# Kernel tuning notes

Hardware: AMD Instinct MI355X
Metric: run time of the kernel (lower is better)

The kernel has to match this reference:

```python
import jax, jax.numpy as jnp
import numpy as np

B, S, H = 2, 2048, 1024
NH, NKV, HD = 16, 16, 64
R, KF = 16, 4
THETA = 1000000.0


def setup_inputs() -> dict:
    key = jax.random.key(0)
    ks = jax.random.split(key, 16)
    sc = 0.02
    signs = jax.random.randint(ks[13], (1, 1, 1, KF, HD // 2), 0, 2).astype(jnp.float32) * 2 - 1
    cdma = jnp.concatenate([signs, signs], axis=-1)  # [1,1,1,KF,HD]
    return {
        "hidden_states": jax.random.normal(ks[0], (B, S, H), jnp.float32),
        "position_ids": jnp.broadcast_to(jnp.arange(S, dtype=jnp.int32), (B, S)),
        "q_w": jax.random.normal(ks[1], (H, H), jnp.float32) * sc,
        "q_b": jax.random.normal(ks[2], (H,), jnp.float32) * sc,
        "k_w": jax.random.normal(ks[3], (H, H), jnp.float32) * sc,
        "k_b": jax.random.normal(ks[4], (H,), jnp.float32) * sc,
        "v_w": jax.random.normal(ks[5], (H, H), jnp.float32) * sc,
        "v_b": jax.random.normal(ks[6], (H,), jnp.float32) * sc,
        "o_w": jax.random.normal(ks[7], (H, H), jnp.float32) * sc,
        "lora_qA": jax.random.normal(ks[8], (R, H), jnp.float32) * sc,
        "lora_qB": jax.random.normal(ks[9], (H, R), jnp.float32) * sc,
        "lora_vA": jax.random.normal(ks[10], (R, H), jnp.float32) * sc,
        "lora_vB": jax.random.normal(ks[11], (H, R), jnp.float32) * sc,
        "cdma_keys": cdma,
    }


def _rope(q, k, position_ids):
    # cos/sin per HF rotary embedding, theta=1e6 (Qwen1.5)
    inv_freq = 1.0 / (THETA ** (jnp.arange(0, HD, 2, dtype=jnp.float32) / HD))  # [HD/2]
    freqs = position_ids.astype(jnp.float32)[..., None] * inv_freq  # [B,S,HD/2]
    emb = jnp.concatenate([freqs, freqs], axis=-1)  # [B,S,HD]
    cos = jnp.cos(emb)[:, None]  # [B,1,S,HD]
    sin = jnp.sin(emb)[:, None]

    def rot_half(x):
        return jnp.concatenate([-x[..., HD // 2:], x[..., :HD // 2]], axis=-1)

    return q * cos + rot_half(q) * sin, k * cos + rot_half(k) * sin


def reference(hidden_states, position_ids, q_w, q_b, k_w, k_b, v_w, v_b, o_w,
              lora_qA, lora_qB, lora_vA, lora_vB, cdma_keys):
    bsz, q_len, _ = hidden_states.shape
    # base projections + LoRA adjustments (k has no LoRA)
    q = hidden_states @ q_w.T + q_b + (hidden_states @ lora_qA.T) @ lora_qB.T
    k = hidden_states @ k_w.T + k_b
    v = hidden_states @ v_w.T + v_b + (hidden_states @ lora_vA.T) @ lora_vB.T

    q = q.reshape(bsz, q_len, NH, HD).transpose(0, 2, 1, 3)   # [B,NH,S,HD]
    k = k.reshape(bsz, q_len, NKV, HD).transpose(0, 2, 1, 3)  # [B,NKV,S,HD]
    v = v.reshape(bsz, q_len, NKV, HD).transpose(0, 2, 1, 3)

    q, k = _rope(q, k, position_ids)

    # holographic block sign-bind/sum transform (q_len divisible by KF -> no pad)
    n_slots = q_len // KF
    k_blocks = k.reshape(bsz, NKV, n_slots, KF, HD)
    v_blocks = v.reshape(bsz, NKV, n_slots, KF, HD)
    S_K = jnp.sum(k_blocks * cdma_keys, axis=3, keepdims=True)  # [B,NKV,slots,1,HD]
    S_V = jnp.sum(v_blocks * cdma_keys, axis=3, keepdims=True)
    K_noisy = (S_K * cdma_keys).reshape(bsz, NKV, q_len, HD)
    V_noisy = (S_V * cdma_keys).reshape(bsz, NKV, q_len, HD)

    scale = 1.0 / (np.sqrt(HD) * np.sqrt(KF))
    scores = jnp.einsum('bhqd,bhkd->bhqk', q, K_noisy) * scale
    causal = jnp.tril(jnp.ones((q_len, q_len), dtype=bool))
    scores = jnp.where(causal, scores, jnp.float32(-1e9))
    attn = jax.nn.softmax(scores, axis=-1)
    out = jnp.einsum('bhqk,bhkd->bhqd', attn, V_noisy)
    out = out.transpose(0, 2, 1, 3).reshape(bsz, q_len, NH * HD)
    return out @ o_w.T
```

## Files before the change

kernel.cpp:

```cpp
#include <hip/hip_runtime.h>
#include <hip/hip_bf16.h>
#include <math.h>


typedef __bf16 bf16;
typedef __attribute__((ext_vector_type(8))) __bf16 bf16x8;
typedef __attribute__((ext_vector_type(4))) float f32x4;

#define NB 2
#define SEQ 2048
#define HID 1024
#define NHD 16
#define HDD 64

__device__ __forceinline__ void gld_lds16(const void* g, void* l) {
  __builtin_amdgcn_global_load_lds(
      (const __attribute__((address_space(1))) void*)g,
      (__attribute__((address_space(3))) void*)l, 16, 0, 0);
}

__device__ __forceinline__ unsigned pack2bf(float a, float b) {
  unsigned short ua = __builtin_bit_cast(unsigned short, (bf16)a);
  unsigned short ub = __builtin_bit_cast(unsigned short, (bf16)b);
  return ((unsigned)ub << 16) | ua;
}

__global__ __launch_bounds__(256) void prep_wqkv(
    const float* __restrict__ qw, const float* __restrict__ kw,
    const float* __restrict__ vw, const float* __restrict__ qA,
    const float* __restrict__ qB, const float* __restrict__ vA,
    const float* __restrict__ vB, bf16* __restrict__ W) {
  int idx = blockIdx.x * 256 + threadIdx.x;
  if (idx >= 3072 * 1024) return;
  int n = idx >> 10, k = idx & 1023;
  float v;
  if (n < 1024) {
    v = qw[n * 1024 + k];
#pragma unroll
    for (int r = 0; r < 16; ++r) v += qB[n * 16 + r] * qA[r * 1024 + k];
  } else if (n < 2048) {
    v = kw[(n - 1024) * 1024 + k];
  } else {
    int nn = n - 2048;
    v = vw[nn * 1024 + k];
#pragma unroll
    for (int r = 0; r < 16; ++r) v += vB[nn * 16 + r] * vA[r * 1024 + k];
  }
  int seg = k >> 6, cl = k & 63;
  int ch = (cl >> 3) ^ (n & 7);
  W[(size_t)n * 1024 + (seg << 6) + (ch << 3) + (cl & 7)] = (bf16)v;
}

__global__ __launch_bounds__(256) void cvt_swz(const float* __restrict__ src,
                                               bf16* __restrict__ dst,
                                               int total, int cols) {
  int idx = blockIdx.x * 256 + threadIdx.x;
  if (idx >= total) return;
  int r = idx / cols, c = idx - r * cols;
  int seg = c >> 6, cl = c & 63;
  int ch = (cl >> 3) ^ (r & 7);
  dst[(size_t)r * cols + (seg << 6) + (ch << 3) + (cl & 7)] = (bf16)src[idx];
}

__global__ void bias_cat(const float* __restrict__ qb, const float* __restrict__ kb,
                         const float* __restrict__ vb, float* __restrict__ out) {
  int i = blockIdx.x * 256 + threadIdx.x;
  if (i >= 3072) return;
  out[i] = (i < 1024) ? qb[i] : (i < 2048 ? kb[i - 1024] : vb[i - 2048]);
}

__global__ void rope_tab(float* __restrict__ ct, float* __restrict__ st) {
  int idx = blockIdx.x * 256 + threadIdx.x;
  if (idx >= SEQ * 32) return;
  int s = idx >> 5, i = idx & 31;
  double inv = pow(1.0e6, -(double)i / 32.0);
  double a = (double)s * inv;
  ct[idx] = (float)cos(a);
  st[idx] = (float)sin(a);
}

__global__ __launch_bounds__(256) void gemm_bt(
    const bf16* __restrict__ A, const bf16* __restrict__ Bw,
    const float* __restrict__ bias, bf16* __restrict__ Cb,
    float* __restrict__ Cf, int M, int N, int K) {
  __shared__ __align__(16) bf16 As[128 * 64];
  __shared__ __align__(16) bf16 Bs[128 * 64];
  const int tid = threadIdx.x;
  const int lane = tid & 63, w = tid >> 6;
  const int wm = w >> 1, wn = w & 1;
  const int l15 = lane & 15, l4 = lane >> 4;
  const int m0 = blockIdx.y * 128, n0 = blockIdx.x * 128;
  const size_t rowb = (size_t)K * 2;
  const char* gA = (const char*)A + (size_t)m0 * rowb;
  const char* gB = (const char*)Bw + (size_t)n0 * rowb;
  f32x4 acc[4][4] = {};

  for (int k0 = 0; k0 < K; k0 += 64) {
    const char* gAk = gA + k0 * 2;
    const char* gBk = gB + k0 * 2;
#pragma unroll
    for (int i = 0; i < 4; ++i) {
      int idx = i * 256 + tid;
      int row = idx >> 3, ch = idx & 7;
      gld_lds16(gAk + (size_t)row * rowb + ch * 16,
                (char*)As + (i * 256 + (w << 6)) * 16);
      gld_lds16(gBk + (size_t)row * rowb + ch * 16,
                (char*)Bs + (i * 256 + (w << 6)) * 16);
    }
    __syncthreads();
#pragma unroll
    for (int c = 0; c < 2; ++c) {
      bf16x8 af[4], bfr[4];
#pragma unroll
      for (int mi = 0; mi < 4; ++mi) {
        int row = wm * 64 + mi * 16 + l15;
        int ch = (c * 4 + l4) ^ (row & 7);
        af[mi] = *(const bf16x8*)(As + row * 64 + ch * 8);
      }
#pragma unroll
      for (int ni = 0; ni < 4; ++ni) {
        int row = wn * 64 + ni * 16 + l15;
        int ch = (c * 4 + l4) ^ (row & 7);
        bfr[ni] = *(const bf16x8*)(Bs + row * 64 + ch * 8);
      }
#pragma unroll
      for (int mi = 0; mi < 4; ++mi)
#pragma unroll
        for (int ni = 0; ni < 4; ++ni)
          acc[mi][ni] = __builtin_amdgcn_mfma_f32_16x16x32_bf16(
              af[mi], bfr[ni], acc[mi][ni], 0, 0, 0);
    }
    __syncthreads();
  }
#pragma unroll
  for (int mi = 0; mi < 4; ++mi) {
    int rbase = m0 + wm * 64 + mi * 16 + l4 * 4;
#pragma unroll
    for (int ni = 0; ni < 4; ++ni) {
      int col = n0 + wn * 64 + ni * 16 + l15;
      float badd = bias ? bias[col] : 0.0f;
#pragma unroll
      for (int r = 0; r < 4; ++r) {
        float v = acc[mi][ni][r] + badd;
        if (Cf) Cf[(size_t)(rbase + r) * N + col] = v;
        else    Cb[(size_t)(rbase + r) * N + col] = (bf16)v;
      }
    }
  }
}

__global__ __launch_bounds__(256) void rope_q(
    const bf16* __restrict__ qkv, const int* __restrict__ pos,
    const float* __restrict__ ct, const float* __restrict__ st,
    bf16* __restrict__ Qr) {
  const float SCQ = 0.0901684403f;
  int idx = blockIdx.x * 256 + threadIdx.x;
  if (idx >= NB * NHD * SEQ * 32) return;
  int i = idx & 31, h = (idx >> 5) & 15, s = (idx >> 9) & 2047, b = idx >> 20;
  int p = pos[b * SEQ + s];
  float co = ct[p * 32 + i], sn = st[p * 32 + i];
  size_t base = ((size_t)(b * SEQ + s)) * 3072 + h * 64 + i;
  float x = (float)qkv[base], y = (float)qkv[base + 32];
  size_t ob = ((size_t)((b * 16 + h) * SEQ + s)) * 64 + i;
  Qr[ob]      = (bf16)((x * co - y * sn) * SCQ);
  Qr[ob + 32] = (bf16)((y * co + x * sn) * SCQ);
}

__global__ __launch_bounds__(256) void holo_kv(
    const bf16* __restrict__ qkv, const int* __restrict__ pos,
    const float* __restrict__ ct, const float* __restrict__ st,
    const float* __restrict__ cdma, bf16* __restrict__ Kn,
    bf16* __restrict__ Vt) {
  int idx = blockIdx.x * 256 + threadIdx.x;
  if (idx >= NB * NHD * (SEQ / 4) * 32) return;
  int i = idx & 31, slot = (idx >> 5) & 511, h = (idx >> 14) & 15, b = idx >> 18;
  float c[4];
  float SK = 0.f, SK2 = 0.f, SV = 0.f, SV2 = 0.f;
#pragma unroll
  for (int f = 0; f < 4; ++f) {
    int s = slot * 4 + f;
    float cf = cdma[f * 64 + i];
    c[f] = cf;
    size_t base = ((size_t)(b * SEQ + s)) * 3072 + h * 64 + i;
    float kx = (float)qkv[base + 1024], ky = (float)qkv[base + 1024 + 32];
    int p = pos[b * SEQ + s];
    float co = ct[p * 32 + i], sn = st[p * 32 + i];
    SK  += (kx * co - ky * sn) * cf;
    SK2 += (ky * co + kx * sn) * cf;
    SV  += (float)qkv[base + 2048] * cf;
    SV2 += (float)qkv[base + 2048 + 32] * cf;
  }
  size_t hb = (size_t)(b * 16 + h);
#pragma unroll
  for (int f = 0; f < 4; ++f) {
    int s = slot * 4 + f;
    size_t krow = (hb * SEQ + s) * 64;
    int ch0 = (i >> 3) ^ (s & 7);
    int ch1 = (4 + (i >> 3)) ^ (s & 7);
    Kn[krow + ch0 * 8 + (i & 7)] = (bf16)(SK * c[f]);
    Kn[krow + ch1 * 8 + (i & 7)] = (bf16)(SK2 * c[f]);
    int seg = s >> 6, cl = s & 63;
    int vch = (cl >> 3) ^ (i & 7);
    size_t vrow0 = (hb * 64 + i) * (size_t)SEQ + (seg << 6);
    size_t vrow1 = (hb * 64 + i + 32) * (size_t)SEQ + (seg << 6);
    Vt[vrow0 + vch * 8 + (cl & 7)] = (bf16)(SV * c[f]);
    Vt[vrow1 + vch * 8 + (cl & 7)] = (bf16)(SV2 * c[f]);
  }
}

__global__ __launch_bounds__(256) void attn_fwd(
    const bf16* __restrict__ Qr, const bf16* __restrict__ Kn,
    const bf16* __restrict__ Vt, bf16* __restrict__ AO) {
  __shared__ __align__(16) bf16 Kt[2][128 * 64];
  __shared__ __align__(16) bf16 Vl[2][64 * 128];
  __shared__ __align__(16) bf16 Pt[4][16 * 128];
  const int pq = blockIdx.x, h = blockIdx.y, b = blockIdx.z;
  const int tid = threadIdx.x, lane = tid & 63, w = tid >> 6;
  const int l15 = lane & 15, l4 = lane >> 4;
  const size_t hd = ((size_t)(b * 16 + h)) * SEQ * 64;
  const char* gK0 = (const char*)(Kn + hd);
  const char* gV0 = (const char*)(Vt + hd);
  char* pw = (char*)&Pt[w][0];

#pragma unroll 1
  for (int phase = 0; phase < 2; ++phase) {
    const int qt = phase ? (31 - pq) : pq;
    const int q0 = qt * 64;
    const int qg = q0 + w * 16 + l15;
    const int nt = (qt >> 1) + 1;

    const bf16* qb = Qr + hd + (size_t)qg * 64;
    bf16x8 qf0 = *(const bf16x8*)(qb + l4 * 8);
    bf16x8 qf1 = *(const bf16x8*)(qb + 32 + l4 * 8);

    f32x4 oacc[4] = {};
    float m = -1e30f, lsum = 0.0f;

#pragma unroll
    for (int i = 0; i < 4; ++i)
      gld_lds16(gK0 + (i * 256 + tid) * 16,
                (char*)Kt[0] + (i * 256 + (w << 6)) * 16);
#pragma unroll
    for (int i = 0; i < 4; ++i) {
      int idx = i * 256 + tid;
      int row = idx >> 4, ch = idx & 15;
      gld_lds16(gV0 + (size_t)row * (SEQ * 2) + ch * 16,
                (char*)Vl[0] + (i * 256 + (w << 6)) * 16);
    }

#pragma unroll 1
    for (int t = 0; t < nt; ++t) {
      const int cur = t & 1;
      if (t + 1 < nt) {
        const int tn = t + 1, sb = cur ^ 1;
#pragma unroll
        for (int i = 0; i < 4; ++i)
          gld_lds16(gK0 + (size_t)tn * 16384 + (i * 256 + tid) * 16,
                    (char*)Kt[sb] + (i * 256 + (w << 6)) * 16);
#pragma unroll
        for (int i = 0; i < 4; ++i) {
          int idx = i * 256 + tid;
          int row = idx >> 4, ch = idx & 15;
          gld_lds16(gV0 + (size_t)row * (SEQ * 2) + tn * 256 + ch * 16,
                    (char*)Vl[sb] + (i * 256 + (w << 6)) * 16);
        }
        asm volatile("s_waitcnt vmcnt(8)\ns_barrier" ::: "memory");
      } else {
        asm volatile("s_waitcnt vmcnt(0)\ns_barrier" ::: "memory");
      }

      const bf16* Ktc = Kt[cur];
      const bf16* Vlc = Vl[cur];
      const int kv0 = t * 128;
      const bool lastt = (t == nt - 1);

      f32x4 sacc[8] = {};
#pragma unroll
      for (int c = 0; c < 2; ++c) {
        bf16x8 qf = c ? qf1 : qf0;
#pragma unroll
        for (int nf = 0; nf < 8; ++nf) {
          int row = nf * 16 + l15;
          int ch = (c * 4 + l4) ^ (row & 7);
          bf16x8 kf = *(const bf16x8*)(Ktc + row * 64 + ch * 8);
          sacc[nf] = __builtin_amdgcn_mfma_f32_16x16x32_bf16(kf, qf, sacc[nf], 0, 0, 0);
        }
      }

      float pmax = -1e30f;
      if (lastt) {
#pragma unroll
        for (int nf = 0; nf < 8; ++nf)
#pragma unroll
          for (int r = 0; r < 4; ++r) {
            int kvg = kv0 + nf * 16 + l4 * 4 + r;
            float v = (kvg > qg) ? -1e30f : sacc[nf][r];
            sacc[nf][r] = v;
            pmax = fmaxf(pmax, v);
          }
      } else {
#pragma unroll
        for (int nf = 0; nf < 8; ++nf)
#pragma unroll
          for (int r = 0; r < 4; ++r) pmax = fmaxf(pmax, sacc[nf][r]);
      }
      pmax = fmaxf(pmax, __shfl_xor(pmax, 16));
      pmax = fmaxf(pmax, __shfl_xor(pmax, 32));

      if (!__all(pmax <= m)) {
        float mn = fmaxf(m, pmax);
        float al = exp2f(m - mn);
        m = mn;
        lsum *= al;
#pragma unroll
        for (int df = 0; df < 4; ++df) oacc[df] *= al;
      }
      float rs = 0.0f;
#pragma unroll
      for (int nf = 0; nf < 8; ++nf)
#pragma unroll
        for (int r = 0; r < 4; ++r) {
          float e = exp2f(sacc[nf][r] - m);
          sacc[nf][r] = e;
          rs += e;
        }
      rs += __shfl_xor(rs, 16);
      rs += __shfl_xor(rs, 32);
      lsum += rs;

#pragma unroll
      for (int nf = 0; nf < 8; ++nf)
#pragma unroll
        for (int rp = 0; rp < 2; ++rp) {
          unsigned u = pack2bf(sacc[nf][rp * 2], sacc[nf][rp * 2 + 1]);
          int boff = l15 * 256 + nf * 32 + l4 * 8 + rp * 4;
          boff ^= (l15 & 7) << 4;
          *(unsigned*)(pw + boff) = u;
        }

#pragma unroll
      for (int c2 = 0; c2 < 4; ++c2) {
        int pb = (l15 * 256 + c2 * 64 + l4 * 16) ^ ((l15 & 7) << 4);
        bf16x8 pf = *(const bf16x8*)(pw + pb);
        int vbyte = (c2 * 64 + l4 * 16) ^ ((l15 & 7) << 4);
#pragma unroll
        for (int df = 0; df < 4; ++df) {
          int vrow = df * 16 + l15;
          bf16x8 vf = *(const bf16x8*)((const char*)Vlc + vrow * 256 + vbyte);
          oacc[df] = __builtin_amdgcn_mfma_f32_16x16x32_bf16(vf, pf, oacc[df], 0, 0, 0);
        }
      }
      asm volatile("s_barrier" ::: "memory");
    }

    const float li = 1.0f / lsum;
    const size_t arow = ((size_t)(b * SEQ + qg)) * HID + h * 64;
    const int qk7 = qg & 7;
#pragma unroll
    for (int df = 0; df < 4; ++df)
#pragma unroll
      for (int r = 0; r < 4; ++r) {
        int d = df * 16 + l4 * 4 + r;
        int ch = (d >> 3) ^ qk7;
        AO[arow + ch * 8 + (d & 7)] = (bf16)(oacc[df][r] * li);
      }
  }
}

extern "C" void kernel_launch(void* const* d_in, const int* in_sizes, int n_in,
                              void* d_out, int out_size, void* d_ws, size_t ws_size,
                              hipStream_t stream) {
  const float* hs  = (const float*)d_in[0];
  const int* pos   = (const int*)d_in[1];
  const float* qw  = (const float*)d_in[2];
  const float* qb_ = (const float*)d_in[3];
  const float* kw  = (const float*)d_in[4];
  const float* kb_ = (const float*)d_in[5];
  const float* vw  = (const float*)d_in[6];
  const float* vb_ = (const float*)d_in[7];
  const float* ow  = (const float*)d_in[8];
  const float* qA  = (const float*)d_in[9];
  const float* qB  = (const float*)d_in[10];
  const float* vA  = (const float*)d_in[11];
  const float* vB  = (const float*)d_in[12];
  const float* cd  = (const float*)d_in[13];

  char* p = (char*)d_ws;
  auto alloc = [&](size_t bytes) {
    char* r = p; p += (bytes + 255) & ~(size_t)255; return r;
  };
  bf16* hsb   = (bf16*)alloc((size_t)4096 * 1024 * 2);
  bf16* Wqkv  = (bf16*)alloc((size_t)3072 * 1024 * 2);
  float* bqkv = (float*)alloc(3072 * 4);
  bf16* owb   = (bf16*)alloc((size_t)1024 * 1024 * 2);
  bf16* qkvb  = (bf16*)alloc((size_t)4096 * 3072 * 2);
  float* ct   = (float*)alloc((size_t)SEQ * 32 * 4);
  float* st   = (float*)alloc((size_t)SEQ * 32 * 4);
  bf16* Qrb   = (bf16*)alloc((size_t)NB * NHD * SEQ * 64 * 2);
  bf16* Knb   = (bf16*)alloc((size_t)NB * NHD * SEQ * 64 * 2);
  bf16* Vtb   = (bf16*)alloc((size_t)NB * NHD * 64 * SEQ * 2);
  bf16* AOb   = (bf16*)alloc((size_t)4096 * 1024 * 2);

  prep_wqkv<<<dim3(3072 * 1024 / 256), 256, 0, stream>>>(qw, kw, vw, qA, qB, vA, vB, Wqkv);
  cvt_swz<<<dim3(4096 * 1024 / 256), 256, 0, stream>>>(hs, hsb, 4096 * 1024, 1024);
  cvt_swz<<<dim3(1024 * 1024 / 256), 256, 0, stream>>>(ow, owb, 1024 * 1024, 1024);
  bias_cat<<<dim3(12), 256, 0, stream>>>(qb_, kb_, vb_, bqkv);
  rope_tab<<<dim3(SEQ * 32 / 256), 256, 0, stream>>>(ct, st);
  gemm_bt<<<dim3(3072 / 128, 4096 / 128), 256, 0, stream>>>(
      hsb, Wqkv, bqkv, qkvb, nullptr, 4096, 3072, 1024);
  rope_q<<<dim3(NB * NHD * SEQ * 32 / 256), 256, 0, stream>>>(qkvb, pos, ct, st, Qrb);
  holo_kv<<<dim3(NB * NHD * (SEQ / 4) * 32 / 256), 256, 0, stream>>>(
      qkvb, pos, ct, st, cd, Knb, Vtb);
  attn_fwd<<<dim3(16, NHD, NB), 256, 0, stream>>>(Qrb, Knb, Vtb, AOb);
  gemm_bt<<<dim3(1024 / 128, 4096 / 128), 256, 0, stream>>>(
      AOb, owb, nullptr, nullptr, (float*)d_out, 4096, 1024, 1024);
}
```

Measured before the change: 166.3 us.

## Merge prep kernels, vectorize rope/holo kernels, split softmax reductions

Folds the five preprocessing kernels (weight merge, two bf16 conversions, bias concat, rope table) into a single launch that branches on block ID. The rope_q and holo_kv kernels now have each thread handle eight contiguous elements with 16-byte bf16x8 loads and stores instead of scalar accesses. In attention, the row max and row sum are accumulated into four independent partials to shorten dependency chains, and probabilities are stored to LDS as 8-byte pairs. The aim is to cut launch overhead and memory-instruction count; the Vt transpose writes stay scalar and strided.

```diff
diff --git a/kernel.cpp b/kernel.cpp
--- a/kernel.cpp
+++ b/kernel.cpp
@@ -6,6 +6,7 @@
 typedef __bf16 bf16;
 typedef __attribute__((ext_vector_type(8))) __bf16 bf16x8;
 typedef __attribute__((ext_vector_type(4))) float f32x4;
+typedef __attribute__((ext_vector_type(2))) unsigned u32x2;
 
 #define NB 2
 #define SEQ 2048
@@ -25,58 +26,65 @@
   return ((unsigned)ub << 16) | ua;
 }
 
-__global__ __launch_bounds__(256) void prep_wqkv(
-    const float* __restrict__ qw, const float* __restrict__ kw,
-    const float* __restrict__ vw, const float* __restrict__ qA,
-    const float* __restrict__ qB, const float* __restrict__ vA,
-    const float* __restrict__ vB, bf16* __restrict__ W) {
-  int idx = blockIdx.x * 256 + threadIdx.x;
-  if (idx >= 3072 * 1024) return;
-  int n = idx >> 10, k = idx & 1023;
-  float v;
-  if (n < 1024) {
-    v = qw[n * 1024 + k];
-#pragma unroll
-    for (int r = 0; r < 16; ++r) v += qB[n * 16 + r] * qA[r * 1024 + k];
-  } else if (n < 2048) {
-    v = kw[(n - 1024) * 1024 + k];
+#define RB_W    12288
+#define RB_HS   (RB_W + 16384)
+#define RB_OW   (RB_HS + 4096)
+#define RB_BIAS (RB_OW + 12)
+#define RB_TAB  (RB_BIAS + 256)
+
+__global__ __launch_bounds__(256) void prep_all(
+    const float* __restrict__ hs, const float* __restrict__ ow,
+    const float* __restrict__ qw, const float* __restrict__ qb,
+    const float* __restrict__ kw, const float* __restrict__ kb,
+    const float* __restrict__ vw, const float* __restrict__ vb,
+    const float* __restrict__ qA, const float* __restrict__ qB,
+    const float* __restrict__ vA, const float* __restrict__ vB,
+    bf16* __restrict__ hsb, bf16* __restrict__ owb, bf16* __restrict__ Wqkv,
+    float* __restrict__ bqkv, float* __restrict__ ct, float* __restrict__ st) {
+  const int bid = blockIdx.x, tid = threadIdx.x;
+  if (bid < RB_W) {
+    int idx = bid * 256 + tid;
+    int n = idx >> 10, k = idx & 1023;
+    float v;
+    if (n < 1024) {
+      v = qw[n * 1024 + k];
+#pragma unroll
+      for (int r = 0; r < 16; ++r) v += qB[n * 16 + r] * qA[r * 1024 + k];
+    } else if (n < 2048) {
+      v = kw[(n - 1024) * 1024 + k];
+    } else {
+      int nn = n - 2048;
+      v = vw[nn * 1024 + k];
+#pragma unroll
+      for (int r = 0; r < 16; ++r) v += vB[nn * 16 + r] * vA[r * 1024 + k];
+    }
+    int seg = k >> 6, cl = k & 63;
+    int ch = (cl >> 3) ^ (n & 7);
+    Wqkv[(size_t)n * 1024 + (seg << 6) + (ch << 3) + (cl & 7)] = (bf16)v;
+  } else if (bid < RB_HS) {
+    int idx = (bid - RB_W) * 256 + tid;
+    int r = idx >> 10, c = idx & 1023;
+    int seg = c >> 6, cl = c & 63;
+    int ch = (cl >> 3) ^ (r & 7);
+    hsb[(size_t)r * 1024 + (seg << 6) + (ch << 3) + (cl & 7)] = (bf16)hs[idx];
+  } else if (bid < RB_OW) {
+    int idx = (bid - RB_HS) * 256 + tid;
+    int r = idx >> 10, c = idx & 1023;
+    int seg = c >> 6, cl = c & 63;
+    int ch = (cl >> 3) ^ (r & 7);
+    owb[(size_t)r * 1024 + (seg << 6) + (ch << 3) + (cl & 7)] = (bf16)ow[idx];
+  } else if (bid < RB_BIAS) {
+    int i = (bid - RB_OW) * 256 + tid;
+    if (i < 3072)
+      bqkv[i] = (i < 1024) ? qb[i] : (i < 2048 ? kb[i - 1024] : vb[i - 2048]);
   } else {
-    int nn = n - 2048;
-    v = vw[nn * 1024 + k];
-#pragma unroll
-    for (int r = 0; r < 16; ++r) v += vB[nn * 16 + r] * vA[r * 1024 + k];
-  }
-  int seg = k >> 6, cl = k & 63;
-  int ch = (cl >> 3) ^ (n & 7);
-  W[(size_t)n * 1024 + (seg << 6) + (ch << 3) + (cl & 7)] = (bf16)v;
-}
-
-__global__ __launch_bounds__(256) void cvt_swz(const float* __restrict__ src,
-                                               bf16* __restrict__ dst,
-                                               int total, int cols) {
-  int idx = blockIdx.x * 256 + threadIdx.x;
-  if (idx >= total) return;
-  int r = idx / cols, c = idx - r * cols;
-  int seg = c >> 6, cl = c & 63;
-  int ch = (cl >> 3) ^ (r & 7);
-  dst[(size_t)r * cols + (seg << 6) + (ch << 3) + (cl & 7)] = (bf16)src[idx];
-}
-
-__global__ void bias_cat(const float* __restrict__ qb, const float* __restrict__ kb,
-                         const float* __restrict__ vb, float* __restrict__ out) {
-  int i = blockIdx.x * 256 + threadIdx.x;
-  if (i >= 3072) return;
-  out[i] = (i < 1024) ? qb[i] : (i < 2048 ? kb[i - 1024] : vb[i - 2048]);
-}
-
-__global__ void rope_tab(float* __restrict__ ct, float* __restrict__ st) {
-  int idx = blockIdx.x * 256 + threadIdx.x;
-  if (idx >= SEQ * 32) return;
-  int s = idx >> 5, i = idx & 31;
-  double inv = pow(1.0e6, -(double)i / 32.0);
-  double a = (double)s * inv;
-  ct[idx] = (float)cos(a);
-  st[idx] = (float)sin(a);
+    int idx = (bid - RB_BIAS) * 256 + tid;
+    int s = idx >> 5, i = idx & 31;
+    double inv = pow(1.0e6, -(double)i / 32.0);
+    double a = (double)s * inv;
+    ct[idx] = (float)cos(a);
+    st[idx] = (float)sin(a);
+  }
 }
 
 __global__ __launch_bounds__(256) void gemm_bt(
@@ -155,15 +163,25 @@
     bf16* __restrict__ Qr) {
   const float SCQ = 0.0901684403f;
   int idx = blockIdx.x * 256 + threadIdx.x;
-  if (idx >= NB * NHD * SEQ * 32) return;
-  int i = idx & 31, h = (idx >> 5) & 15, s = (idx >> 9) & 2047, b = idx >> 20;
+  if (idx >= NB * NHD * SEQ * 4) return;
+  int ih = idx & 3, s = (idx >> 2) & 2047, h = (idx >> 13) & 15, b = idx >> 17;
   int p = pos[b * SEQ + s];
-  float co = ct[p * 32 + i], sn = st[p * 32 + i];
-  size_t base = ((size_t)(b * SEQ + s)) * 3072 + h * 64 + i;
-  float x = (float)qkv[base], y = (float)qkv[base + 32];
-  size_t ob = ((size_t)((b * 16 + h) * SEQ + s)) * 64 + i;
-  Qr[ob]      = (bf16)((x * co - y * sn) * SCQ);
-  Qr[ob + 32] = (bf16)((y * co + x * sn) * SCQ);
+  size_t base = ((size_t)(b * SEQ + s)) * 3072 + h * 64 + ih * 8;
+  bf16x8 xv = *(const bf16x8*)(qkv + base);
+  bf16x8 yv = *(const bf16x8*)(qkv + base + 32);
+  const float* ctp = ct + p * 32 + ih * 8;
+  const float* stp = st + p * 32 + ih * 8;
+  bf16x8 o0, o1;
+#pragma unroll
+  for (int e = 0; e < 8; ++e) {
+    float x = (float)xv[e], y = (float)yv[e];
+    float co = ctp[e], sn = stp[e];
+    o0[e] = (bf16)((x * co - y * sn) * SCQ);
+    o1[e] = (bf16)((y * co + x * sn) * SCQ);
+  }
+  size_t ob = ((size_t)((b * 16 + h) * SEQ + s)) * 64 + ih * 8;
+  *(bf16x8*)(Qr + ob) = o0;
+  *(bf16x8*)(Qr + ob + 32) = o1;
 }
 
 __global__ __launch_bounds__(256) void holo_kv(
@@ -172,39 +190,57 @@
     const float* __restrict__ cdma, bf16* __restrict__ Kn,
     bf16* __restrict__ Vt) {
   int idx = blockIdx.x * 256 + threadIdx.x;
-  if (idx >= NB * NHD * (SEQ / 4) * 32) return;
-  int i = idx & 31, slot = (idx >> 5) & 511, h = (idx >> 14) & 15, b = idx >> 18;
-  float c[4];
-  float SK = 0.f, SK2 = 0.f, SV = 0.f, SV2 = 0.f;
+  if (idx >= NB * NHD * (SEQ / 4) * 4) return;
+  int ih = idx & 3, slot = (idx >> 2) & 511, h = (idx >> 11) & 15, b = idx >> 15;
+  float SK[8] = {}, SK2[8] = {}, SV[8] = {}, SV2[8] = {};
 #pragma unroll
   for (int f = 0; f < 4; ++f) {
     int s = slot * 4 + f;
-    float cf = cdma[f * 64 + i];
-    c[f] = cf;
-    size_t base = ((size_t)(b * SEQ + s)) * 3072 + h * 64 + i;
-    float kx = (float)qkv[base + 1024], ky = (float)qkv[base + 1024 + 32];
+    size_t base = ((size_t)(b * SEQ + s)) * 3072 + h * 64 + ih * 8;
+    bf16x8 klo = *(const bf16x8*)(qkv + base + 1024);
+    bf16x8 khi = *(const bf16x8*)(qkv + base + 1024 + 32);
+    bf16x8 vlo = *(const bf16x8*)(qkv + base + 2048);
+    bf16x8 vhi = *(const bf16x8*)(qkv + base + 2048 + 32);
     int p = pos[b * SEQ + s];
-    float co = ct[p * 32 + i], sn = st[p * 32 + i];
-    SK  += (kx * co - ky * sn) * cf;
-    SK2 += (ky * co + kx * sn) * cf;
-    SV  += (float)qkv[base + 2048] * cf;
-    SV2 += (float)qkv[base + 2048 + 32] * cf;
+    const float* ctp = ct + p * 32 + ih * 8;
+    const float* stp = st + p * 32 + ih * 8;
+    const float* cdp = cdma + f * 64 + ih * 8;
+#pragma unroll
+    for (int e = 0; e < 8; ++e) {
+      float cf = cdp[e];
+      float kx = (float)klo[e], ky = (float)khi[e];
+      float co = ctp[e], sn = stp[e];
+      SK[e]  += (kx * co - ky * sn) * cf;
+      SK2[e] += (ky * co + kx * sn) * cf;
+      SV[e]  += (float)vlo[e] * cf;
+      SV2[e] += (float)vhi[e] * cf;
+    }
   }
   size_t hb = (size_t)(b * 16 + h);
 #pragma unroll
   for (int f = 0; f < 4; ++f) {
     int s = slot * 4 + f;
+    const float* cdp = cdma + f * 64 + ih * 8;
+    bf16x8 k0, k1;
+#pragma unroll
+    for (int e = 0; e < 8; ++e) {
+      k0[e] = (bf16)(SK[e] * cdp[e]);
+      k1[e] = (bf16)(SK2[e] * cdp[e]);
+    }
     size_t krow = (hb * SEQ + s) * 64;
-    int ch0 = (i >> 3) ^ (s & 7);
-    int ch1 = (4 + (i >> 3)) ^ (s & 7);
-    Kn[krow + ch0 * 8 + (i & 7)] = (bf16)(SK * c[f]);
-    Kn[krow + ch1 * 8 + (i & 7)] = (bf16)(SK2 * c[f]);
+    int ch0 = ih ^ (s & 7);
+    int ch1 = (4 + ih) ^ (s & 7);
+    *(bf16x8*)(Kn + krow + ch0 * 8) = k0;
+    *(bf16x8*)(Kn + krow + ch1 * 8) = k1;
     int seg = s >> 6, cl = s & 63;
-    int vch = (cl >> 3) ^ (i & 7);
-    size_t vrow0 = (hb * 64 + i) * (size_t)SEQ + (seg << 6);
-    size_t vrow1 = (hb * 64 + i + 32) * (size_t)SEQ + (seg << 6);
-    Vt[vrow0 + vch * 8 + (cl & 7)] = (bf16)(SV * c[f]);
-    Vt[vrow1 + vch * 8 + (cl & 7)] = (bf16)(SV2 * c[f]);
+    size_t vcol = (size_t)(seg << 6) + (cl & 7);
+#pragma unroll
+    for (int e = 0; e < 8; ++e) {
+      int i = ih * 8 + e;
+      int vch = (cl >> 3) ^ (i & 7);
+      Vt[(hb * 64 + i) * (size_t)SEQ + vcol + vch * 8] = (bf16)(SV[e] * cdp[e]);
+      Vt[(hb * 64 + i + 32) * (size_t)SEQ + vcol + vch * 8] = (bf16)(SV2[e] * cdp[e]);
+    }
   }
 }
 
@@ -287,7 +323,7 @@
         }
       }
 
-      float pmax = -1e30f;
+      float px[4] = {-1e30f, -1e30f, -1e30f, -1e30f};
       if (lastt) {
 #pragma unroll
         for (int nf = 0; nf < 8; ++nf)
@@ -296,14 +332,15 @@
             int kvg = kv0 + nf * 16 + l4 * 4 + r;
             float v = (kvg > qg) ? -1e30f : sacc[nf][r];
             sacc[nf][r] = v;
-            pmax = fmaxf(pmax, v);
+            px[nf & 3] = fmaxf(px[nf & 3], v);
           }
       } else {
 #pragma unroll
         for (int nf = 0; nf < 8; ++nf)
 #pragma unroll
-          for (int r = 0; r < 4; ++r) pmax = fmaxf(pmax, sacc[nf][r]);
-      }
+          for (int r = 0; r < 4; ++r) px[nf & 3] = fmaxf(px[nf & 3], sacc[nf][r]);
+      }
+      float pmax = fmaxf(fmaxf(px[0], px[1]), fmaxf(px[2], px[3]));
       pmax = fmaxf(pmax, __shfl_xor(pmax, 16));
       pmax = fmaxf(pmax, __shfl_xor(pmax, 32));
 
@@ -315,28 +352,28 @@
 #pragma unroll
         for (int df = 0; df < 4; ++df) oacc[df] *= al;
       }
-      float rs = 0.0f;
+      float rs4[4] = {0.f, 0.f, 0.f, 0.f};
 #pragma unroll
       for (int nf = 0; nf < 8; ++nf)
 #pragma unroll
         for (int r = 0; r < 4; ++r) {
           float e = exp2f(sacc[nf][r] - m);
           sacc[nf][r] = e;
-          rs += e;
+          rs4[nf & 3] += e;
         }
+      float rs = (rs4[0] + rs4[1]) + (rs4[2] + rs4[3]);
       rs += __shfl_xor(rs, 16);
       rs += __shfl_xor(rs, 32);
       lsum += rs;
 
 #pragma unroll
-      for (int nf = 0; nf < 8; ++nf)
-#pragma unroll
-        for (int rp = 0; rp < 2; ++rp) {
-          unsigned u = pack2bf(sacc[nf][rp * 2], sacc[nf][rp * 2 + 1]);
-          int boff = l15 * 256 + nf * 32 + l4 * 8 + rp * 4;
-          boff ^= (l15 & 7) << 4;
-          *(unsigned*)(pw + boff) = u;
-        }
+      for (int nf = 0; nf < 8; ++nf) {
+        u32x2 u;
+        u.x = pack2bf(sacc[nf][0], sacc[nf][1]);
+        u.y = pack2bf(sacc[nf][2], sacc[nf][3]);
+        int boff = (l15 * 256 + nf * 32 + l4 * 8) ^ ((l15 & 7) << 4);
+        *(u32x2*)(pw + boff) = u;
+      }
 
 #pragma unroll
       for (int c2 = 0; c2 < 4; ++c2) {
@@ -401,15 +438,13 @@
   bf16* Vtb   = (bf16*)alloc((size_t)NB * NHD * 64 * SEQ * 2);
   bf16* AOb   = (bf16*)alloc((size_t)4096 * 1024 * 2);
 
-  prep_wqkv<<<dim3(3072 * 1024 / 256), 256, 0, stream>>>(qw, kw, vw, qA, qB, vA, vB, Wqkv);
-  cvt_swz<<<dim3(4096 * 1024 / 256), 256, 0, stream>>>(hs, hsb, 4096 * 1024, 1024);
-  cvt_swz<<<dim3(1024 * 1024 / 256), 256, 0, stream>>>(ow, owb, 1024 * 1024, 1024);
-  bias_cat<<<dim3(12), 256, 0, stream>>>(qb_, kb_, vb_, bqkv);
-  rope_tab<<<dim3(SEQ * 32 / 256), 256, 0, stream>>>(ct, st);
+  prep_all<<<dim3(RB_TAB), 256, 0, stream>>>(
+      hs, ow, qw, qb_, kw, kb_, vw, vb_, qA, qB, vA, vB,
+      hsb, owb, Wqkv, bqkv, ct, st);
   gemm_bt<<<dim3(3072 / 128, 4096 / 128), 256, 0, stream>>>(
       hsb, Wqkv, bqkv, qkvb, nullptr, 4096, 3072, 1024);
-  rope_q<<<dim3(NB * NHD * SEQ * 32 / 256), 256, 0, stream>>>(qkvb, pos, ct, st, Qrb);
-  holo_kv<<<dim3(NB * NHD * (SEQ / 4) * 32 / 256), 256, 0, stream>>>(
+  rope_q<<<dim3(NB * NHD * SEQ * 4 / 256), 256, 0, stream>>>(qkvb, pos, ct, st, Qrb);
+  holo_kv<<<dim3(NB * NHD * (SEQ / 4) * 4 / 256), 256, 0, stream>>>(
       qkvb, pos, ct, st, cd, Knb, Vtb);
   attn_fwd<<<dim3(16, NHD, NB), 256, 0, stream>>>(Qrb, Knb, Vtb, AOb);
   gemm_bt<<<dim3(1024 / 128, 4096 / 128), 256, 0, stream>>>(
```

New measurement: 158.2 us. 4.9% less time.
